# Kernel tuning notes

Hardware: AMD Instinct MI355X
Metric: run time of the kernel (lower is better)

Reference implementation:

```python
import jax, jax.numpy as jnp
import numpy as np

K = 5
BASE_LAMBDA = 0.05
BASE_DELTA = 0.01
TV_ITERS = 3
TV_STEP = 0.2
LAMBDA_RANGE = (0.5, 1.5)
JITTER = 0.1
FUSION_SCALE = 2.0
BETA_T = 0.02
BETA_S = 0.01
BETA_MIN = 0.0
BETA_MAX = 1.0
EPS = 1e-8


def _gen_param_sets():
    # Deterministic replication of SGSv2Config._generate_param_sets
    rng = np.random.RandomState(0)
    ps = [(0.0, 0.0, 0, 0.0)]
    lmin = BASE_LAMBDA * LAMBDA_RANGE[0]
    lmax = BASE_LAMBDA * LAMBDA_RANGE[1]
    for i in range(K - 1):
        lb = lmin + (lmax - lmin) * i / max(1, K - 2)
        jit = rng.uniform(-JITTER, JITTER)
        li = max(0.0, lb * (1 + jit))
        di = BASE_DELTA * float(np.sqrt(li / (BASE_LAMBDA + 1e-8)))
        ps.append((float(li), di, TV_ITERS, TV_STEP))
    return ps

PARAM_SETS = _gen_param_sets()


def lower_median(v, axis):
    # torch.median semantics: lower of the two middle values for even n
    s = jnp.sort(v, axis=axis)
    n = v.shape[axis]
    return jnp.take(s, (n - 1) // 2, axis=axis)


def huber_tv(x, lam, delta, iters, step):
    # Anisotropic Huber-TV, skip_clamp=True (artifact path)
    xd = x
    for _ in range(iters):
        dx = jnp.pad(xd[:, :, :, 1:] - xd[:, :, :, :-1], ((0, 0), (0, 0), (0, 0), (0, 1)))
        dy = jnp.pad(xd[:, :, 1:, :] - xd[:, :, :-1, :], ((0, 0), (0, 0), (0, 1), (0, 0)))
        gx = dx / (delta + jnp.abs(dx))
        gy = dy / (delta + jnp.abs(dy))
        div_x = gx - jnp.pad(gx[:, :, :, :-1], ((0, 0), (0, 0), (0, 0), (1, 0)))
        div_y = gy - jnp.pad(gy[:, :, :-1, :], ((0, 0), (0, 0), (1, 0), (0, 0)))
        xd = xd - step * (xd - x - lam * (div_x + div_y))
    return xd


def setup_inputs() -> dict:
    key = jax.random.key(0)
    x = jax.random.normal(key, (32, 3, 256, 256), dtype=jnp.float32)
    return {"x": x}


def reference(x):
    B = x.shape[0]
    # per-sample artifact scale: median of |x| over (C,H,W)
    scale = lower_median(jnp.abs(x).reshape(B, -1), axis=1).reshape(B, 1, 1, 1) + EPS
    x_norm = x / scale
    views = [x]
    for k in range(1, K):
        lam, delta, iters, step = PARAM_SETS[k]
        views.append(huber_tv(x_norm, lam, delta, iters, step) * scale)
    stack = jnp.stack(views, axis=0)  # [K,B,C,H,W]
    med = lower_median(stack, axis=0)  # K odd -> true median
    dev = jnp.abs(stack - med[None])
    mad = lower_median(dev, axis=0)
    mad = jnp.maximum(mad, 0.1 * mad.mean())
    w = jnp.exp(-dev / (FUSION_SCALE * mad[None]))
    fused = (w * stack).sum(axis=0) / (w.sum(axis=0) + EPS)
    # adaptive beta (corruption detection)
    D = dev.mean(axis=(0, 2, 3, 4)).reshape(-1, 1, 1, 1)
    beta = BETA_MIN + (BETA_MAX - BETA_MIN) * jax.nn.sigmoid((D - BETA_T) / BETA_S)
    return fused, beta
```

## Files before the change

### kernel.cpp

```cpp
#include <hip/hip_runtime.h>
#include <hip/hip_fp16.h>
#include <math.h>

#define B_ 32
#define C_ 3
#define H_ 256
#define W_ 256
#define HW_ 65536
#define CHW_ 196608
#define TOT_ 6291456

#define VIEWS_OFF_B 0ull
#define GHIST_OFF_B (4ull * TOT_ * 2ull)
#define STATE_OFF_B (GHIST_OFF_B + 32ull*2048*4)
#define SCALE_OFF_B (STATE_OFF_B + 32ull*8)
#define PMAD_OFF_B  (SCALE_OFF_B + 32ull*4)
#define PDEV_OFF_B  (PMAD_OFF_B + 1536ull*4)

#define RC_ 32
#define RB5_ 5
#define NW_ 8
#define NBAND_ 8

__device__ __forceinline__ float g_of(float d, float delta) {
    return d * __builtin_amdgcn_rcpf(delta + fabsf(d));
}
__device__ __forceinline__ void cswap(float& a, float& b) {
    float lo = fminf(a, b), hi = fmaxf(a, b); a = lo; b = hi;
}
__device__ __forceinline__ float median5(float a0, float a1, float a2, float a3, float a4) {
    cswap(a0,a1); cswap(a3,a4); cswap(a2,a4); cswap(a2,a3); cswap(a0,a3);
    cswap(a0,a2); cswap(a1,a4); cswap(a1,a3); cswap(a1,a2);
    return a2;
}

__device__ __forceinline__ float4 loadv4(const __half* p) {
    union { float2 f; __half2 h[2]; } u;
    u.f = *(const float2*)p;
    float2 lo = __half22float2(u.h[0]), hi = __half22float2(u.h[1]);
    return make_float4(lo.x, lo.y, hi.x, hi.y);
}

__global__ __launch_bounds__(256) void k_init(unsigned* state, unsigned* ghist) {
    int t = threadIdx.x, s = blockIdx.x;
    #pragma unroll
    for (int i = 0; i < 8; i++) ghist[s*2048 + t + 256*i] = 0u;
    if (t == 0) { state[2*s] = 0u; state[2*s+1] = 98303u; }
}

__global__ __launch_bounds__(256) void k_hist(const float* __restrict__ x,
                                              unsigned* __restrict__ ghist,
                                              const unsigned* __restrict__ state,
                                              unsigned matchmask, int shift) {
    __shared__ unsigned h[2048];
    int t = threadIdx.x, chunk = blockIdx.x, s = blockIdx.y;
    #pragma unroll
    for (int i = 0; i < 8; i++) h[t + 256*i] = 0u;
    __syncthreads();
    unsigned prefix = state[2*s];
    size_t base = (size_t)s*CHW_ + (size_t)chunk*4096;
    #pragma unroll
    for (int i = 0; i < 16; i++) {
        float v = x[base + i*256 + t];
        unsigned u = __float_as_uint(fabsf(v));
        if ((u & matchmask) == prefix) atomicAdd(&h[(u >> shift) & 2047u], 1u);
    }
    __syncthreads();
    #pragma unroll
    for (int i = 0; i < 8; i++) {
        unsigned c = h[t + 256*i];
        if (c) atomicAdd(&ghist[s*2048 + t + 256*i], c);
    }
}

__global__ __launch_bounds__(256) void k_select(unsigned* __restrict__ ghist,
                                                unsigned* __restrict__ state,
                                                float* __restrict__ scale,
                                                int shift, int final_pass, unsigned mid) {
    __shared__ unsigned sc[256];
    int t = threadIdx.x, s = blockIdx.x;
    unsigned krem = state[2*s+1];
    unsigned v[8]; unsigned ts = 0;
    #pragma unroll
    for (int i = 0; i < 8; i++) { v[i] = ghist[s*2048 + t*8 + i]; ts += v[i]; }
    sc[t] = ts; __syncthreads();
    for (int off = 1; off < 256; off <<= 1) {
        unsigned a = sc[t];
        unsigned b = (t >= off) ? sc[t-off] : 0u;
        __syncthreads();
        sc[t] = a + b;
        __syncthreads();
    }
    unsigned incl = sc[t], base = incl - ts;
    if (ts > 0 && base <= krem && krem < incl) {
        unsigned c = base; int dig = -1; unsigned nk = 0;
        #pragma unroll
        for (int i = 0; i < 8; i++) {
            if (dig < 0) {
                if (krem < c + v[i]) { dig = t*8 + i; nk = krem - c; }
                else c += v[i];
            }
        }
        unsigned prefix = state[2*s] | ((unsigned)dig << shift);
        state[2*s] = prefix;
        state[2*s+1] = nk;
        if (final_pass) scale[s] = __uint_as_float(prefix | mid) + 1e-8f;
    }
    #pragma unroll
    for (int i = 0; i < 8; i++) ghist[s*2048 + t*8 + i] = 0u;
}

#define LDXNQ(r) loadv4(&xnl[wr0 + (r)][col])

#define STEP(r, nxt) { \
    float4 a = s##r; float4 vn = nxt; \
    float vn3 = __shfl_down(a.x, 1); \
    float g0 = g_of(a.y - a.x, del); \
    float g1 = g_of(a.z - a.y, del); \
    float g2 = g_of(a.w - a.z, del); \
    float g3 = g_of(vn3 - a.w, del); g3 = is63 ? 0.f : g3; \
    float gxl = __shfl_up(g3, 1); gxl = is0 ? 0.f : gxl; \
    float4 gy; gy.x = g_of(vn.x - a.x, del); gy.y = g_of(vn.y - a.y, del); \
    gy.z = g_of(vn.z - a.z, del); gy.w = g_of(vn.w - a.w, del); \
    float4 xq = LDXNQ(r); \
    a.x = fmaf(lam02, (g0 - gxl) + (gy.x - gprev.x), fmaf(0.8f, a.x, xq.x)); \
    a.y = fmaf(lam02, (g1 - g0)  + (gy.y - gprev.y), fmaf(0.8f, a.y, xq.y)); \
    a.z = fmaf(lam02, (g2 - g1)  + (gy.z - gprev.z), fmaf(0.8f, a.z, xq.z)); \
    a.w = fmaf(lam02, (g3 - g2)  + (gy.w - gprev.w), fmaf(0.8f, a.w, xq.w)); \
    s##r = a; gprev = gy; }

#define LDXN5(r) (make_float4(5.f*LDXNQ(r).x, 5.f*LDXNQ(r).y, 5.f*LDXNQ(r).z, 5.f*LDXNQ(r).w))

#define STOREROW5(r) { int wr = wr0 + r; \
    if (wr >= 4 && wr < 4 + RC_) { int gi = i0 + wr - 4; \
        union { __half2 h[2]; float2 f; } pk; \
        pk.h[0] = __floats2half2_rn(s##r.x, s##r.y); \
        pk.h[1] = __floats2half2_rn(s##r.z, s##r.w); \
        *(float2*)(vout + (size_t)gi*W_ + col) = pk.f; } }

__global__ __launch_bounds__(512) void k_views(const float* __restrict__ x,
        __half* __restrict__ views, const float* __restrict__ scale,
        float l0, float l1, float l2, float l3,
        float e0, float e1, float e2, float e3) {
    __shared__ __align__(16) __half xnl[40][256];
    __shared__ float exch[2][NW_][2][256];
    const int t = threadIdx.x, lane = t & 63, wv = t >> 6;
    const int band = blockIdx.x, bc = blockIdx.y, b = bc / 3;
    const int i0 = band * RC_;
    const float sc = scale[b];
    const float* img = x + (size_t)bc * HW_;
    const int wr0 = wv * RB5_, col = lane << 2;
    const bool topblk = (band == 0), botblk = (band == NBAND_ - 1);
    const bool is0 = (lane == 0), is63 = (lane == 63);

    #pragma unroll
    for (int r = 0; r < RB5_; r++) {
        int gi = i0 - 4 + wr0 + r; gi = gi < 0 ? 0 : (gi > 255 ? 255 : gi);
        float4 v = *(const float4*)(img + gi * W_ + col);
        union { __half2 h[2]; float2 f; } pk;
        pk.h[0] = __floats2half2_rn(0.2f * v.x, 0.2f * v.y);
        pk.h[1] = __floats2half2_rn(0.2f * v.z, 0.2f * v.w);
        *(float2*)&xnl[wr0 + r][col] = pk.f;
    }
    __syncthreads();

    float4 s0, s1, s2, s3, s4, gt, gb;

    #pragma unroll 1
    for (int view = 0; view < 4; view++) {
        const float lamv = (view == 0) ? l0 : (view == 1) ? l1 : (view == 2) ? l2 : l3;
        const float delv = (view == 0) ? e0 : (view == 1) ? e1 : (view == 2) ? e2 : e3;
        const float del = delv * sc;
        const float lam02 = 0.2f * lamv * sc;
        s0 = LDXN5(0); s1 = LDXN5(1); s2 = LDXN5(2); s3 = LDXN5(3); s4 = LDXN5(4);
        gt = (wv == 0)       ? s0 : LDXN5(-1);
        gb = (wv == NW_ - 1) ? s4 : LDXN5(5);

        #pragma unroll 1
        for (int it = 0; it < 3; it++) {
            float4 gprev;
            gprev.x = g_of(s0.x - gt.x, del);
            gprev.y = g_of(s0.y - gt.y, del);
            gprev.z = g_of(s0.z - gt.z, del);
            gprev.w = g_of(s0.w - gt.w, del);
            STEP(0, s1) STEP(1, s2) STEP(2, s3) STEP(3, s4) STEP(4, gb)
            if (it < 2) {
                *(float4*)&exch[it][wv][0][col] = s0;
                *(float4*)&exch[it][wv][1][col] = s4;
                __syncthreads();
                gt = wv ? *(const float4*)&exch[it][wv - 1][1][col] : s0;
                gb = (wv < NW_ - 1) ? *(const float4*)&exch[it][wv + 1][0][col] : s4;
                if (topblk && wv == 0)       { s0 = s4; s1 = s4; s2 = s4; s3 = s4; gt = s4; }
                if (botblk && wv == NW_ - 1) { s1 = s0; s2 = s0; s3 = s0; s4 = s0; gb = s0; }
            }
        }
        __half* vout = views + (size_t)view * TOT_ + (size_t)bc * HW_;
        STOREROW5(0) STOREROW5(1) STOREROW5(2) STOREROW5(3) STOREROW5(4)
    }
}

__global__ __launch_bounds__(256) void k_stats(const float* __restrict__ x,
                                               const __half* __restrict__ views,
                                               float* __restrict__ pmad,
                                               float* __restrict__ pdev) {
    int t = threadIdx.x, chunk = blockIdx.x, b = blockIdx.y;
    float am = 0.f, ad = 0.f;
    #pragma unroll
    for (int i = 0; i < 4; i++) {
        size_t px = (size_t)b*CHW_ + ((size_t)chunk*1024 + i*256 + t) * 4;
        float4 a0 = *(const float4*)(x + px);
        float4 a1 = loadv4(views + px);
        float4 a2 = loadv4(views + TOT_ + px);
        float4 a3 = loadv4(views + 2ull*TOT_ + px);
        float4 a4 = loadv4(views + 3ull*TOT_ + px);
        const float* q0 = &a0.x; const float* q1 = &a1.x; const float* q2 = &a2.x;
        const float* q3 = &a3.x; const float* q4 = &a4.x;
        #pragma unroll
        for (int j = 0; j < 4; j++) {
            float s0 = q0[j], s1 = q1[j], s2 = q2[j], s3 = q3[j], s4 = q4[j];
            float med = median5(s0, s1, s2, s3, s4);
            float d0 = fabsf(s0-med), d1 = fabsf(s1-med), d2 = fabsf(s2-med),
                  d3 = fabsf(s3-med), d4 = fabsf(s4-med);
            am += median5(d0, d1, d2, d3, d4);
            ad += d0 + d1 + d2 + d3 + d4;
        }
    }
    __shared__ float r[256];
    r[t] = am; __syncthreads();
    for (int off = 128; off > 0; off >>= 1) { if (t < off) r[t] += r[t+off]; __syncthreads(); }
    if (t == 0) pmad[b*48 + chunk] = r[0];
    __syncthreads();
    r[t] = ad; __syncthreads();
    for (int off = 128; off > 0; off >>= 1) { if (t < off) r[t] += r[t+off]; __syncthreads(); }
    if (t == 0) pdev[b*48 + chunk] = r[0];
}

__global__ __launch_bounds__(256) void k_fuse(const float* __restrict__ x,
                                              const __half* __restrict__ views,
                                              const float* __restrict__ pmad,
                                              const float* __restrict__ pdev,
                                              float* __restrict__ out) {
    int t = threadIdx.x;
    __shared__ float rr[256];
    float sm = 0.f;
    for (int j = t; j < 1536; j += 256) sm += pmad[j];
    rr[t] = sm; __syncthreads();
    for (int off = 128; off > 0; off >>= 1) { if (t < off) rr[t] += rr[t+off]; __syncthreads(); }
    float floorv = 0.1f * (rr[0] / (float)TOT_);
    __syncthreads();

    if (blockIdx.x == 0 && t < 32) {
        float sd = 0.f;
        for (int j = 0; j < 48; j++) sd += pdev[t*48 + j];
        float D = sd / (5.0f * (float)CHW_);
        float z = (D - 0.02f) / 0.01f;
        out[TOT_ + t] = 1.0f / (1.0f + __expf(-z));
    }

    for (int i = 0; i < 16; i++) {
        size_t px = ((size_t)blockIdx.x*4096 + i*256 + t) * 4;
        float4 a0 = *(const float4*)(x + px);
        float4 a1 = loadv4(views + px);
        float4 a2 = loadv4(views + TOT_ + px);
        float4 a3 = loadv4(views + 2ull*TOT_ + px);
        float4 a4 = loadv4(views + 3ull*TOT_ + px);
        const float* q0 = &a0.x; const float* q1 = &a1.x; const float* q2 = &a2.x;
        const float* q3 = &a3.x; const float* q4 = &a4.x;
        float4 o;
        float* qo = &o.x;
        #pragma unroll
        for (int j = 0; j < 4; j++) {
            float s0 = q0[j], s1 = q1[j], s2 = q2[j], s3 = q3[j], s4 = q4[j];
            float med = median5(s0, s1, s2, s3, s4);
            float d0 = fabsf(s0-med), d1 = fabsf(s1-med), d2 = fabsf(s2-med),
                  d3 = fabsf(s3-med), d4 = fabsf(s4-med);
            float mad = median5(d0, d1, d2, d3, d4);
            float madf = fmaxf(mad, floorv);
            float inv = 1.0f / (2.0f * madf);
            float w0 = __expf(-d0*inv), w1 = __expf(-d1*inv), w2 = __expf(-d2*inv),
                  w3 = __expf(-d3*inv), w4 = __expf(-d4*inv);
            float num = w0*s0 + w1*s1 + w2*s2 + w3*s3 + w4*s4;
            float den = w0 + w1 + w2 + w3 + w4 + 1e-8f;
            qo[j] = num / den;
        }
        *(float4*)(out + px) = o;
    }
}

extern "C" void kernel_launch(void* const* d_in, const int* in_sizes, int n_in,
                              void* d_out, int out_size, void* d_ws, size_t ws_size,
                              hipStream_t stream) {
    const float* x = (const float*)d_in[0];
    float* out = (float*)d_out;
    char* ws = (char*)d_ws;
    __half*   views = (__half*)(ws + VIEWS_OFF_B);
    unsigned* ghist = (unsigned*)(ws + GHIST_OFF_B);
    unsigned* state = (unsigned*)(ws + STATE_OFF_B);
    float*    scale = (float*)(ws + SCALE_OFF_B);
    float*    pmad  = (float*)(ws + PMAD_OFF_B);
    float*    pdev  = (float*)(ws + PDEV_OFF_B);

    const double s4h[4] = {0.5488135039273248, 0.7151893663724195,
                           0.6027633760716439, 0.5448831829968969};
    float lam[4], del[4];
    for (int i = 0; i < 4; i++) {
        double lb  = 0.025 + (0.075 - 0.025) * (double)i / 3.0;
        double jit = -0.1 + 0.2 * s4h[i];
        double li  = lb * (1.0 + jit);
        if (li < 0.0) li = 0.0;
        double di  = 0.01 * sqrt(li / (0.05 + 1e-8));
        lam[i] = (float)li; del[i] = (float)di;
    }

    k_init<<<32, 256, 0, stream>>>(state, ghist);

    k_hist  <<<dim3(48,32), 256, 0, stream>>>(x, ghist, state, 0u,          21);
    k_select<<<32,          256, 0, stream>>>(ghist, state, scale, 21, 0, 0u);
    k_hist  <<<dim3(48,32), 256, 0, stream>>>(x, ghist, state, 0xFFE00000u, 10);
    k_select<<<32,          256, 0, stream>>>(ghist, state, scale, 10, 1, 0x200u);

    k_views<<<dim3(NBAND_,96), 512, 0, stream>>>(x, views, scale,
                                                 lam[0], lam[1], lam[2], lam[3],
                                                 del[0], del[1], del[2], del[3]);
    k_stats<<<dim3(48,32), 256, 0, stream>>>(x, views, pmad, pdev);
    k_fuse <<<384,         256, 0, stream>>>(x, views, pmad, pdev, out);
    (void)in_sizes; (void)n_in; (void)out_size; (void)ws_size;
}
```

Measured before the change: 132.8 us.

## Shrink TV row bands to 16 rows with 3 rows per wave and half-precision halo exchange

```diff
diff --git a/kernel.cpp b/kernel.cpp
--- a/kernel.cpp
+++ b/kernel.cpp
@@ -17,10 +17,10 @@
 #define PMAD_OFF_B  (SCALE_OFF_B + 32ull*4)
 #define PDEV_OFF_B  (PMAD_OFF_B + 1536ull*4)
 
-#define RC_ 32
-#define RB5_ 5
+#define RC_ 16
+#define RB3_ 3
 #define NW_ 8
-#define NBAND_ 8
+#define NBAND_ 16
 
 __device__ __forceinline__ float g_of(float d, float delta) {
     return d * __builtin_amdgcn_rcpf(delta + fabsf(d));
@@ -39,6 +39,12 @@
     u.f = *(const float2*)p;
     float2 lo = __half22float2(u.h[0]), hi = __half22float2(u.h[1]);
     return make_float4(lo.x, lo.y, hi.x, hi.y);
+}
+__device__ __forceinline__ void storev4(__half* p, float4 v) {
+    union { float2 f; __half2 h[2]; } u;
+    u.h[0] = __floats2half2_rn(v.x, v.y);
+    u.h[1] = __floats2half2_rn(v.z, v.w);
+    *(float2*)p = u.f;
 }
 
 __global__ __launch_bounds__(256) void k_init(unsigned* state, unsigned* ghist) {
@@ -131,40 +137,35 @@
 
 #define LDXN5(r) (make_float4(5.f*LDXNQ(r).x, 5.f*LDXNQ(r).y, 5.f*LDXNQ(r).z, 5.f*LDXNQ(r).w))
 
-#define STOREROW5(r) { int wr = wr0 + r; \
+#define STOREROW3(r) { int wr = wr0 + r; \
     if (wr >= 4 && wr < 4 + RC_) { int gi = i0 + wr - 4; \
-        union { __half2 h[2]; float2 f; } pk; \
-        pk.h[0] = __floats2half2_rn(s##r.x, s##r.y); \
-        pk.h[1] = __floats2half2_rn(s##r.z, s##r.w); \
-        *(float2*)(vout + (size_t)gi*W_ + col) = pk.f; } }
+        storev4(vout + (size_t)gi*W_ + col, s##r); } }
 
 __global__ __launch_bounds__(512) void k_views(const float* __restrict__ x,
         __half* __restrict__ views, const float* __restrict__ scale,
         float l0, float l1, float l2, float l3,
         float e0, float e1, float e2, float e3) {
-    __shared__ __align__(16) __half xnl[40][256];
-    __shared__ float exch[2][NW_][2][256];
+    __shared__ __align__(16) __half xnl[24][256];
+    __shared__ __align__(16) __half exch[NW_][2][256];
     const int t = threadIdx.x, lane = t & 63, wv = t >> 6;
     const int band = blockIdx.x, bc = blockIdx.y, b = bc / 3;
     const int i0 = band * RC_;
     const float sc = scale[b];
     const float* img = x + (size_t)bc * HW_;
-    const int wr0 = wv * RB5_, col = lane << 2;
+    const int wr0 = wv * RB3_, col = lane << 2;
     const bool topblk = (band == 0), botblk = (band == NBAND_ - 1);
     const bool is0 = (lane == 0), is63 = (lane == 63);
 
     #pragma unroll
-    for (int r = 0; r < RB5_; r++) {
+    for (int r = 0; r < RB3_; r++) {
         int gi = i0 - 4 + wr0 + r; gi = gi < 0 ? 0 : (gi > 255 ? 255 : gi);
         float4 v = *(const float4*)(img + gi * W_ + col);
-        union { __half2 h[2]; float2 f; } pk;
-        pk.h[0] = __floats2half2_rn(0.2f * v.x, 0.2f * v.y);
-        pk.h[1] = __floats2half2_rn(0.2f * v.z, 0.2f * v.w);
-        *(float2*)&xnl[wr0 + r][col] = pk.f;
-    }
-    __syncthreads();
-
-    float4 s0, s1, s2, s3, s4, gt, gb;
+        v.x *= 0.2f; v.y *= 0.2f; v.z *= 0.2f; v.w *= 0.2f;
+        storev4(&xnl[wr0 + r][col], v);
+    }
+    __syncthreads();
+
+    float4 s0, s1, s2, gt, gb;
 
     #pragma unroll 1
     for (int view = 0; view < 4; view++) {
@@ -172,9 +173,9 @@
         const float delv = (view == 0) ? e0 : (view == 1) ? e1 : (view == 2) ? e2 : e3;
         const float del = delv * sc;
         const float lam02 = 0.2f * lamv * sc;
-        s0 = LDXN5(0); s1 = LDXN5(1); s2 = LDXN5(2); s3 = LDXN5(3); s4 = LDXN5(4);
+        s0 = LDXN5(0); s1 = LDXN5(1); s2 = LDXN5(2);
         gt = (wv == 0)       ? s0 : LDXN5(-1);
-        gb = (wv == NW_ - 1) ? s4 : LDXN5(5);
+        gb = (wv == NW_ - 1) ? s2 : LDXN5(3);
 
         #pragma unroll 1
         for (int it = 0; it < 3; it++) {
@@ -183,19 +184,23 @@
             gprev.y = g_of(s0.y - gt.y, del);
             gprev.z = g_of(s0.z - gt.z, del);
             gprev.w = g_of(s0.w - gt.w, del);
-            STEP(0, s1) STEP(1, s2) STEP(2, s3) STEP(3, s4) STEP(4, gb)
+            STEP(0, s1) STEP(1, s2) STEP(2, gb)
             if (it < 2) {
-                *(float4*)&exch[it][wv][0][col] = s0;
-                *(float4*)&exch[it][wv][1][col] = s4;
+                if (topblk && wv == 1) s0 = s1;
+                if (botblk && wv == NW_ - 2) s2 = s1;
                 __syncthreads();
-                gt = wv ? *(const float4*)&exch[it][wv - 1][1][col] : s0;
-                gb = (wv < NW_ - 1) ? *(const float4*)&exch[it][wv + 1][0][col] : s4;
-                if (topblk && wv == 0)       { s0 = s4; s1 = s4; s2 = s4; s3 = s4; gt = s4; }
-                if (botblk && wv == NW_ - 1) { s1 = s0; s2 = s0; s3 = s0; s4 = s0; gb = s0; }
+                storev4(&exch[wv][0][col], s0);
+                storev4(&exch[wv][1][col], s2);
+                __syncthreads();
+                gt = wv ? loadv4(&exch[wv - 1][1][col]) : s0;
+                gb = (wv < NW_ - 1) ? loadv4(&exch[wv + 1][0][col]) : s2;
+                if (topblk && wv == 0)       { s0 = gb; s1 = gb; s2 = gb; gt = gb; }
+                if (botblk && wv == NW_ - 1) { s0 = gt; s1 = gt; s2 = gt; gb = gt; }
             }
         }
         __half* vout = views + (size_t)view * TOT_ + (size_t)bc * HW_;
-        STOREROW5(0) STOREROW5(1) STOREROW5(2) STOREROW5(3) STOREROW5(4)
+        STOREROW3(0) STOREROW3(1) STOREROW3(2)
+        if (view < 3) __syncthreads();
     }
 }
 
```

Measured after the change: 147.4 us. +11.0%, slower.
